# Performance work log

Measured on AMD Instinct MI355X. Metric: run time of the kernel, lower is better.

Reference implementation:

```python
import jax, jax.numpy as jnp
import numpy as np
from math import sqrt

RATIOS = [0.5, 1.0, 2.0]
SCALES = [128.0, 256.0, 512.0]
STRIDE = 16
NA = 9  # len(RATIOS) * len(SCALES)


def _anchor_template():
    # matches RPNHead.__init__: center at stride/2, w = s/sqrt(r), h = s*sqrt(r)
    t = np.zeros((NA, 4), np.float32)
    for ri, r in enumerate(RATIOS):
        for si, s in enumerate(SCALES):
            i = ri * len(RATIOS) + si
            sr = sqrt(r)
            t[i] = [STRIDE / 2.0, STRIDE / 2.0, s / sr, s * sr]
    return jnp.asarray(t)


def _conv(x, w, b, pad):
    y = jax.lax.conv_general_dilated(
        x, w, window_strides=(1, 1), padding=[(pad, pad), (pad, pad)],
        dimension_numbers=('NCHW', 'OIHW', 'NCHW'))
    return y + b[None, :, None, None]


def setup_inputs() -> dict:
    key = jax.random.key(0)
    ks = jax.random.split(key, 5)
    B, C, H, W = 8, 512, 64, 64
    return {
        'feature_maps': jax.random.normal(ks[0], (B, C, H, W), jnp.float32),
        'img_size': jnp.ones((B, 2), jnp.int32) * 1024,  # (width, height) per image
        'conv_w': jax.random.normal(ks[1], (512, 512, 3, 3), jnp.float32) * 0.01,
        'conv_b': jnp.zeros((512,), jnp.float32),
        'cls_w': jax.random.normal(ks[2], (2 * NA, 512, 1, 1), jnp.float32) * 0.01,
        'cls_b': jnp.zeros((2 * NA,), jnp.float32),
        'reg_w': jax.random.normal(ks[3], (4 * NA, 512, 1, 1), jnp.float32) * 0.01,
        'reg_b': jnp.zeros((4 * NA,), jnp.float32),
    }


def reference(feature_maps, img_size, conv_w, conv_b, cls_w, cls_b, reg_w, reg_b):
    f = jax.nn.relu(_conv(feature_maps, conv_w, conv_b, 1))  # [B,512,H,W]
    B, _, H, W = f.shape
    # heads, NCHW -> NHWC, split anchor dim
    cls = _conv(f, cls_w, cls_b, 0).transpose(0, 2, 3, 1).reshape(B, H, W, NA, 2)
    reg = _conv(f, reg_w, reg_b, 0).transpose(0, 2, 3, 1).reshape(B, H, W, NA, 4)

    # generate_anchors (eval mode: anchors_ignore stays zero)
    tmpl = _anchor_template()  # [NA,4] xywh
    gy, gx = jnp.meshgrid(jnp.arange(H), jnp.arange(W), indexing='ij')
    center = jnp.stack([gx, gy], axis=-1).astype(jnp.float32) * STRIDE  # [H,W,2] (x,y)
    axy = tmpl[None, None, :, :2] + center[:, :, None, :]               # [H,W,NA,2]
    awh = jnp.broadcast_to(tmpl[None, None, :, 2:], (H, W, NA, 2))
    anchors = jnp.concatenate([axy, awh], axis=-1).reshape(-1, 4)       # [A,4]

    A = anchors.shape[0]
    reg = reg.reshape(B, A, 4)
    cls_scores = cls.reshape(B, A, 2)

    # anchor2bbox: inverse of the delta encoding in loss()
    ax, ay, aw, ah = anchors[:, 0], anchors[:, 1], anchors[:, 2], anchors[:, 3]
    px = ax[None, :] + reg[..., 0] * aw[None, :]
    py = ay[None, :] + reg[..., 1] * ah[None, :]
    pw = aw[None, :] * jnp.exp(reg[..., 2])
    ph = ah[None, :] * jnp.exp(reg[..., 3])
    imw = img_size[:, 0:1].astype(jnp.float32)
    imh = img_size[:, 1:2].astype(jnp.float32)
    x1 = jnp.clip(px - pw / 2, 0.0, imw)
    y1 = jnp.clip(py - ph / 2, 0.0, imh)
    x2 = jnp.clip(px + pw / 2, 0.0, imw)
    y2 = jnp.clip(py + ph / 2, 0.0, imh)
    proposals = jnp.stack([x1, y1, x2, y2], axis=-1)  # [B,A,4]

    anchors_ignore = jnp.zeros((B, A), jnp.int32)
    return (proposals, cls_scores, anchors_ignore)
```

## Files before the change

kernel.cpp:

```cpp
#include <hip/hip_runtime.h>
#include <hip/hip_bf16.h>
#include <stdint.h>

typedef __attribute__((ext_vector_type(4))) float f32x4;
typedef __attribute__((ext_vector_type(8))) short short8;

#define NB 8
#define NC 512
#define HP 66
#define WP 66
#define NPOS 32768
#define KTOT 4608
#define NKT 72

#define XP_ELEMS (NB*HP*WP*NC)
#define WR_ELEMS (NC*KTOT)
#define WC2_ELEMS (64*NC)
#define PROP_OFF 0
#define CLS_OFF  1179648
#define ANCH_OFF 1769472
#define A_PER_B  36864

__device__ __forceinline__ short bf16bits(float v) {
    __hip_bfloat16 b = __float2bfloat16(v);
    return *reinterpret_cast<short*>(&b);
}
__device__ __forceinline__ void gload16(const short* g, short* l) {
    __builtin_amdgcn_global_load_lds(
        (const __attribute__((address_space(1))) unsigned int*)g,
        (__attribute__((address_space(3))) unsigned int*)l, 16, 0, 0);
}
#define BARRIER() asm volatile("s_barrier" ::: "memory")
#define VMCNT4()  asm volatile("s_waitcnt vmcnt(4)" ::: "memory")
#define VMCNT0()  asm volatile("s_waitcnt vmcnt(0)" ::: "memory")

__global__ void prep_all(const float* __restrict__ x, const float* __restrict__ conv_w,
                         const float* __restrict__ cls_w, const float* __restrict__ reg_w,
                         short* __restrict__ Wr, short* __restrict__ Wc2,
                         short* __restrict__ Xp) {
    __shared__ float smem[4608];
    const int bid = blockIdx.x, tid = threadIdx.x;
    if (bid < 4096) {
        float (*t)[65] = (float(*)[65])smem;
        const int pb = bid & 63, cb = (bid >> 6) & 7, b = bid >> 9;
        const int tx = tid & 63, ty = tid >> 6;
        const float* src = x + ((size_t)(b*NC + cb*64))*4096 + pb*64;
#pragma unroll
        for (int r = 0; r < 16; ++r) {
            int ch = ty + r*4;
            t[ch][tx] = src[(size_t)ch*4096 + tx];
        }
        __syncthreads();
#pragma unroll
        for (int rr = 0; rr < 2; ++rr) {
            int item = tid + rr*256;
            int pl = item >> 3, ck = item & 7;
            short8 v;
#pragma unroll
            for (int e = 0; e < 8; ++e) v[e] = bf16bits(t[ck*8+e][pl]);
            *(short8*)&Xp[((size_t)((b*HP + pb + 1)*WP) + (pl + 1))*NC + cb*64 + ck*8] = v;
        }
    } else if (bid < 4608) {
        const int o = bid - 4096;
        const float* src = conv_w + (size_t)o*4608;
        for (int i = tid; i < 4608; i += 256) smem[i] = src[i];
        __syncthreads();
#pragma unroll
        for (int k = 0; k < 9; ++k)
#pragma unroll
            for (int c = 0; c < 2; ++c) {
                int ci = tid + c*256;
                Wr[(size_t)o*4608 + k*512 + ci] = bf16bits(smem[ci*9 + k]);
            }
    } else {
        const int m = bid - 4608;
        if (m < 128) {
            int t = m*256 + tid;
            int row = t >> 9, ci = t & 511;
            float v = 0.f;
            if (row < 18)      v = cls_w[row*NC + ci];
            else if (row < 54) v = reg_w[(row-18)*NC + ci];
            Wc2[t] = bf16bits(v);
        } else {
            int idx = (m-128)*256 + tid;
            int b = idx / 16640;
            int rem = idx - b*16640;
            int r = rem >> 6, g = rem & 63;
            int h, w;
            if      (r < 66)  { h = 0;       w = r; }
            else if (r < 132) { h = 65;      w = r - 66; }
            else if (r < 196) { h = r - 131; w = 0; }
            else              { h = r - 195; w = 65; }
            short8 z = (short8){0,0,0,0,0,0,0,0};
            *(short8*)&Xp[((size_t)((b*HP + h)*WP) + w)*NC + g*8] = z;
        }
    }
}

__launch_bounds__(512, 2)
__global__ void conv_fused(const short* __restrict__ Xp, const short* __restrict__ Wr,
                           const float* __restrict__ bias, const short* __restrict__ Wc2,
                           float* __restrict__ partial) {
    extern __shared__ short lds[];
    const int tid = threadIdx.x;
    const int lane = tid & 63, wv = tid >> 6;
    const int bid = blockIdx.x;
    const int wg = (bid & 7) * 32 + (bid >> 3);
    const int pbase  = (wg >> 1) * 256;
    const int cobase = (wg & 1) * 256;
    const int wm = wv >> 2, wn = wv & 3;

    const int g_data = (tid & 7) ^ ((tid >> 3) & 7);
    int abase[4], bbase[4];
#pragma unroll
    for (int q = 0; q < 4; ++q) {
        int p = pbase + q*64 + (tid >> 3);
        int b = p >> 12, h = (p >> 6) & 63, w = p & 63;
        abase[q] = ((b*HP + h)*WP + w)*NC + g_data*8;
        bbase[q] = (cobase + q*64 + (tid >> 3))*KTOT + g_data*8;
    }
    const int stoff = tid*8;

    const int l15 = lane & 15, l4 = lane >> 4, l7 = lane & 7;
    const int kidx0 = (l4 ^ l7) * 8;
    const int kidx1 = ((4 + l4) ^ l7) * 8;
    const int Aroff = wm*8192 + l15*64;
    const int Broff = 16384 + (wn>>1)*8192 + (wn&1)*4096 + l15*64;

    auto stageA = [&](int t, int hh) {
        int seg = t >> 3;
        int dh = seg / 3, dw = seg - dh*3;
        int off = (dh*WP + dw)*NC + (t & 7)*64;
        short* dst = lds + (t & 1)*32768 + hh*8192 + stoff;
        gload16(Xp + abase[hh*2+0] + off, dst);
        gload16(Xp + abase[hh*2+1] + off, dst + 4096);
    };
    auto stageB = [&](int t, int hh) {
        int off = t * 64;
        short* dst = lds + (t & 1)*32768 + 16384 + hh*8192 + stoff;
        gload16(Wr + bbase[hh*2+0] + off, dst);
        gload16(Wr + bbase[hh*2+1] + off, dst + 4096);
    };

    f32x4 acc[8][4];
#pragma unroll
    for (int i = 0; i < 8; ++i)
#pragma unroll
        for (int j = 0; j < 4; ++j) acc[i][j] = (f32x4){0.f,0.f,0.f,0.f};

    short8 af[2][2], bfr[4][2];
    auto readA = [&](int bufb, int i2) {
        const short* Ab = lds + bufb*32768 + Aroff;
#pragma unroll
        for (int ii = 0; ii < 2; ++ii) {
            af[ii][0] = *(const short8*)(Ab + (i2+ii)*1024 + kidx0);
            af[ii][1] = *(const short8*)(Ab + (i2+ii)*1024 + kidx1);
        }
    };
    auto readB = [&](int bufb) {
        const short* Bb = lds + bufb*32768 + Broff;
#pragma unroll
        for (int j = 0; j < 4; ++j) {
            bfr[j][0] = *(const short8*)(Bb + j*1024 + kidx0);
            bfr[j][1] = *(const short8*)(Bb + j*1024 + kidx1);
        }
    };
    auto mfmaQ = [&](int i2) {
        __builtin_amdgcn_s_setprio(1);
#pragma unroll
        for (int kk = 0; kk < 2; ++kk)
#pragma unroll
            for (int ii = 0; ii < 2; ++ii)
#pragma unroll
                for (int j = 0; j < 4; ++j)
                    acc[i2+ii][j] = __builtin_amdgcn_mfma_f32_16x16x32_bf16(
                        af[ii][kk], bfr[j][kk], acc[i2+ii][j], 0, 0, 0);
        __builtin_amdgcn_s_setprio(0);
    };

    stageB(0,0); stageB(0,1); stageA(0,0); stageA(0,1); stageB(1,0); stageB(1,1);
    VMCNT4(); BARRIER();

    for (int it = 0; it < 36; ++it) {
        const int t1 = 2*it+1, t2 = 2*it+2, t3 = 2*it+3;
        const bool s2 = (t2 < NKT), s3 = (t3 < NKT);
        readB(0); readA(0, 0);
        stageA(t1, 0);
        BARRIER(); mfmaQ(0); BARRIER();
        readA(0, 2);
        stageA(t1, 1);
        BARRIER(); mfmaQ(2); BARRIER();
        readA(0, 4);
        if (s2) stageB(t2, 0);
        BARRIER(); mfmaQ(4); BARRIER();
        readA(0, 6);
        if (s2) stageB(t2, 1);
        BARRIER(); mfmaQ(6);
        if (s2) { VMCNT4(); } else { VMCNT0(); }
        BARRIER();
        readB(1); readA(1, 0);
        if (s2) stageA(t2, 0);
        BARRIER(); mfmaQ(0); BARRIER();
        readA(1, 2);
        if (s2) stageA(t2, 1);
        BARRIER(); mfmaQ(2); BARRIER();
        readA(1, 4);
        if (s3) stageB(t3, 0);
        BARRIER(); mfmaQ(4); BARRIER();
        readA(1, 6);
        if (s3) stageB(t3, 1);
        BARRIER(); mfmaQ(6);
        if (s3) { VMCNT4(); } else { VMCNT0(); }
        BARRIER();
    }
    __syncthreads();

#pragma unroll
    for (int j = 0; j < 4; ++j) {
        const int ch = wn*64 + j*16 + l15;
        const float bb = bias[cobase + ch];
        const int g = ch >> 3, e = ch & 7;
#pragma unroll
        for (int i = 0; i < 8; ++i) {
#pragma unroll
            for (int r = 0; r < 4; ++r) {
                const int pos = wm*128 + i*16 + l4*4 + r;
                float v = acc[i][j][r] + bb;
                v = v > 0.f ? v : 0.f;
                const int slot = (g & 24) | ((g ^ pos) & 7);
                lds[pos*256 + slot*8 + e] = bf16bits(v);
            }
        }
    }
    __syncthreads();

    f32x4 acc2[2][4];
#pragma unroll
    for (int i2 = 0; i2 < 2; ++i2)
#pragma unroll
        for (int j2 = 0; j2 < 4; ++j2) acc2[i2][j2] = (f32x4){0.f,0.f,0.f,0.f};
    const int hbase = wv*32;
#pragma unroll
    for (int kk = 0; kk < 8; ++kk) {
        short8 b2[4];
#pragma unroll
        for (int j2 = 0; j2 < 4; ++j2)
            b2[j2] = *(const short8*)&Wc2[(size_t)(j2*16 + l15)*NC + cobase + kk*32 + l4*8];
#pragma unroll
        for (int i2 = 0; i2 < 2; ++i2) {
            const int pos = hbase + i2*16 + l15;
            const int g = kk*4 + l4;
            const int slot = (g & 24) | ((g ^ pos) & 7);
            short8 a2 = *(const short8*)&lds[pos*256 + slot*8];
#pragma unroll
            for (int j2 = 0; j2 < 4; ++j2)
                acc2[i2][j2] = __builtin_amdgcn_mfma_f32_16x16x32_bf16(
                    a2, b2[j2], acc2[i2][j2], 0, 0, 0);
        }
    }

    const int half = wg & 1;
    float* pdst = partial + ((size_t)half*NPOS + pbase + hbase)*64;
#pragma unroll
    for (int i2 = 0; i2 < 2; ++i2)
#pragma unroll
        for (int j2 = 0; j2 < 4; ++j2)
#pragma unroll
            for (int r = 0; r < 4; ++r)
                pdst[(i2*16 + l4*4 + r)*64 + j2*16 + l15] = acc2[i2][j2][r];
}

__device__ const float AW_T[9] = {
    181.01933598375618f, 362.03867196751236f, 724.0773439350247f,
    128.f, 256.f, 512.f,
    90.50966799187809f, 181.01933598375618f, 362.03867196751236f };
__device__ const float AH_T[9] = {
    90.50966799187809f, 181.01933598375618f, 362.03867196751236f,
    128.f, 256.f, 512.f,
    181.01933598375618f, 362.03867196751236f, 724.0773439350247f };

__launch_bounds__(256)
__global__ void combine_decode(const float* __restrict__ partial,
                               const float* __restrict__ cls_b, const float* __restrict__ reg_b,
                               const int* __restrict__ img, float* __restrict__ out) {
    __shared__ float sm[64*65];
    const int tid = threadIdx.x;
    const int p0 = blockIdx.x * 64;
    const float4* pa = (const float4*)partial;
#pragma unroll
    for (int q = 0; q < 4; ++q) {
        int idx = tid + q*256;
        int pl = idx >> 4, n4 = idx & 15;
        float4 a = pa[(size_t)(p0 + pl)*16 + n4];
        float4 b = pa[(size_t)(NPOS + p0 + pl)*16 + n4];
        sm[pl*65 + n4*4 + 0] = a.x + b.x;
        sm[pl*65 + n4*4 + 1] = a.y + b.y;
        sm[pl*65 + n4*4 + 2] = a.z + b.z;
        sm[pl*65 + n4*4 + 3] = a.w + b.w;
    }
    __syncthreads();

    for (int item = tid; item < 576; item += 256) {
        int pl = item / 9, a = item - pl*9;
        int p = p0 + pl;
        int b = p >> 12, h = (p >> 6) & 63, w = p & 63;
        float c0 = sm[pl*65 + a*2 + 0] + cls_b[a*2 + 0];
        float c1 = sm[pl*65 + a*2 + 1] + cls_b[a*2 + 1];
        float r0 = sm[pl*65 + 18 + a*4 + 0] + reg_b[a*4 + 0];
        float r1 = sm[pl*65 + 18 + a*4 + 1] + reg_b[a*4 + 1];
        float r2 = sm[pl*65 + 18 + a*4 + 2] + reg_b[a*4 + 2];
        float r3 = sm[pl*65 + 18 + a*4 + 3] + reg_b[a*4 + 3];
        float aw = AW_T[a], ah = AH_T[a];
        float ax = 8.f + 16.f*w, ay = 8.f + 16.f*h;
        float px = ax + r0*aw,  py = ay + r1*ah;
        float pw = aw*__expf(r2), ph = ah*__expf(r3);
        float imw = (float)img[b*2 + 0], imh = (float)img[b*2 + 1];
        float x1 = fminf(fmaxf(px - 0.5f*pw, 0.f), imw);
        float y1 = fminf(fmaxf(py - 0.5f*ph, 0.f), imh);
        float x2 = fminf(fmaxf(px + 0.5f*pw, 0.f), imw);
        float y2 = fminf(fmaxf(py + 0.5f*ph, 0.f), imh);
        int ag = (h*64 + w)*9 + a;
        float4* prop = (float4*)(out + PROP_OFF + ((size_t)b*A_PER_B + ag)*4);
        *prop = make_float4(x1, y1, x2, y2);
        float2* cs = (float2*)(out + CLS_OFF + ((size_t)b*A_PER_B + ag)*2);
        *cs = make_float2(c0, c1);
        out[ANCH_OFF + (size_t)b*A_PER_B + ag] = 0.0f;
    }
}

extern "C" void kernel_launch(void* const* d_in, const int* in_sizes, int n_in,
                              void* d_out, int out_size, void* d_ws, size_t ws_size,
                              hipStream_t stream) {
    const float* x      = (const float*)d_in[0];
    const int*   img    = (const int*)  d_in[1];
    const float* conv_w = (const float*)d_in[2];
    const float* conv_b = (const float*)d_in[3];
    const float* cls_w  = (const float*)d_in[4];
    const float* cls_b  = (const float*)d_in[5];
    const float* reg_w  = (const float*)d_in[6];
    const float* reg_b  = (const float*)d_in[7];
    float* out = (float*)d_out;

    short* Xp      = (short*)d_ws;
    short* Wr      = Xp  + XP_ELEMS;
    short* Wc2     = Wr  + WR_ELEMS;
    float* partial = (float*)(Wc2 + WC2_ELEMS);

    prep_all<<<5256, 256, 0, stream>>>(x, conv_w, cls_w, reg_w, Wr, Wc2, Xp);

    hipFuncSetAttribute((const void*)conv_fused,
                        hipFuncAttributeMaxDynamicSharedMemorySize, 131072);
    conv_fused<<<256, 512, 131072, stream>>>(Xp, Wr, conv_b, Wc2, partial);
    combine_decode<<<NPOS/64, 256, 0, stream>>>(partial, cls_b, reg_b, img, out);
}
```

Baseline: 248.1 us.

## Merge prep, conv and decode into one cooperative persistent kernel with grid syncs

Replaces the three separate launches (prep, fused conv, combine/decode) with a single cooperative kernel of 256 workgroups that runs the three phases back to back, separated by grid-wide syncs. The prep phase is reworked so each 512-thread block runs two 256-thread teams over the transpose and weight-reorder jobs, and the input reads become float4 loads. The aim is to remove launch overhead and the gaps between kernels. In exchange, prep and decode now run on only 256 large workgroups at low occupancy, and the kernel pays for two grid barriers.

```diff
diff --git a/kernel.cpp b/kernel.cpp
--- a/kernel.cpp
+++ b/kernel.cpp
@@ -1,6 +1,9 @@
 #include <hip/hip_runtime.h>
 #include <hip/hip_bf16.h>
+#include <hip/hip_cooperative_groups.h>
 #include <stdint.h>
+
+namespace cg = cooperative_groups;
 
 typedef __attribute__((ext_vector_type(4))) float f32x4;
 typedef __attribute__((ext_vector_type(8))) short short8;
@@ -20,6 +23,7 @@
 #define CLS_OFF  1179648
 #define ANCH_OFF 1769472
 #define A_PER_B  36864
+#define TSTRIDE  4672
 
 __device__ __forceinline__ short bf16bits(float v) {
     __hip_bfloat16 b = __float2bfloat16(v);
@@ -34,55 +38,86 @@
 #define VMCNT4()  asm volatile("s_waitcnt vmcnt(4)" ::: "memory")
 #define VMCNT0()  asm volatile("s_waitcnt vmcnt(0)" ::: "memory")
 
-__global__ void prep_all(const float* __restrict__ x, const float* __restrict__ conv_w,
-                         const float* __restrict__ cls_w, const float* __restrict__ reg_w,
-                         short* __restrict__ Wr, short* __restrict__ Wc2,
-                         short* __restrict__ Xp) {
-    __shared__ float smem[4608];
-    const int bid = blockIdx.x, tid = threadIdx.x;
-    if (bid < 4096) {
-        float (*t)[65] = (float(*)[65])smem;
-        const int pb = bid & 63, cb = (bid >> 6) & 7, b = bid >> 9;
-        const int tx = tid & 63, ty = tid >> 6;
-        const float* src = x + ((size_t)(b*NC + cb*64))*4096 + pb*64;
-#pragma unroll
-        for (int r = 0; r < 16; ++r) {
-            int ch = ty + r*4;
-            t[ch][tx] = src[(size_t)ch*4096 + tx];
-        }
-        __syncthreads();
-#pragma unroll
-        for (int rr = 0; rr < 2; ++rr) {
-            int item = tid + rr*256;
-            int pl = item >> 3, ck = item & 7;
-            short8 v;
-#pragma unroll
-            for (int e = 0; e < 8; ++e) v[e] = bf16bits(t[ck*8+e][pl]);
-            *(short8*)&Xp[((size_t)((b*HP + pb + 1)*WP) + (pl + 1))*NC + cb*64 + ck*8] = v;
-        }
-    } else if (bid < 4608) {
-        const int o = bid - 4096;
-        const float* src = conv_w + (size_t)o*4608;
-        for (int i = tid; i < 4608; i += 256) smem[i] = src[i];
-        __syncthreads();
-#pragma unroll
-        for (int k = 0; k < 9; ++k)
-#pragma unroll
-            for (int c = 0; c < 2; ++c) {
-                int ci = tid + c*256;
-                Wr[(size_t)o*4608 + k*512 + ci] = bf16bits(smem[ci*9 + k]);
+__device__ const float AW_T[9] = {
+    181.01933598375618f, 362.03867196751236f, 724.0773439350247f,
+    128.f, 256.f, 512.f,
+    90.50966799187809f, 181.01933598375618f, 362.03867196751236f };
+__device__ const float AH_T[9] = {
+    90.50966799187809f, 181.01933598375618f, 362.03867196751236f,
+    128.f, 256.f, 512.f,
+    181.01933598375618f, 362.03867196751236f, 724.0773439350247f };
+
+__launch_bounds__(512, 2)
+__global__ void mega(const float* __restrict__ x, const int* __restrict__ img,
+                     const float* __restrict__ conv_w, const float* __restrict__ bias,
+                     const float* __restrict__ cls_w, const float* __restrict__ cls_b,
+                     const float* __restrict__ reg_w, const float* __restrict__ reg_b,
+                     float* __restrict__ out, short* __restrict__ Xp,
+                     short* __restrict__ Wr, short* __restrict__ Wc2,
+                     float* __restrict__ partial) {
+    extern __shared__ short lds[];
+    cg::grid_group gg = cg::this_grid();
+    const int tid = threadIdx.x;
+    const int bid = blockIdx.x;
+
+    {
+        const int team = tid >> 8, ttid = tid & 255;
+        float* tsm = (float*)lds + team*TSTRIDE;
+        float (*t65)[65] = (float(*)[65])tsm;
+
+#pragma unroll 1
+        for (int r = 0; r < 8; ++r) {
+            const int job = bid*16 + r*2 + team;
+            const int pb = job & 63, cb = (job >> 6) & 7, b = job >> 9;
+            const float* src = x + ((size_t)(b*NC + cb*64))*4096 + pb*64;
+            const int w4 = ttid & 15, chb = ttid >> 4;
+#pragma unroll
+            for (int r2 = 0; r2 < 4; ++r2) {
+                int ch = r2*16 + chb;
+                float4 v = *(const float4*)(src + (size_t)ch*4096 + w4*4);
+                t65[ch][w4*4 + 0] = v.x;
+                t65[ch][w4*4 + 1] = v.y;
+                t65[ch][w4*4 + 2] = v.z;
+                t65[ch][w4*4 + 3] = v.w;
             }
-    } else {
-        const int m = bid - 4608;
-        if (m < 128) {
-            int t = m*256 + tid;
+            __syncthreads();
+#pragma unroll
+            for (int rr = 0; rr < 2; ++rr) {
+                int item = ttid + rr*256;
+                int pl = item >> 3, ck = item & 7;
+                short8 v;
+#pragma unroll
+                for (int e = 0; e < 8; ++e) v[e] = bf16bits(t65[ck*8+e][pl]);
+                *(short8*)&Xp[((size_t)((b*HP + pb + 1)*WP) + (pl + 1))*NC + cb*64 + ck*8] = v;
+            }
+            __syncthreads();
+        }
+
+        {
+            const int o = bid*2 + team;
+            const float4* src4 = (const float4*)(conv_w + (size_t)o*4608);
+            float4* tsm4 = (float4*)tsm;
+            for (int i = ttid; i < 1152; i += 256) tsm4[i] = src4[i];
+            __syncthreads();
+#pragma unroll
+            for (int k = 0; k < 9; ++k)
+#pragma unroll
+                for (int c = 0; c < 2; ++c) {
+                    int ci = ttid + c*256;
+                    Wr[(size_t)o*4608 + k*512 + ci] = bf16bits(tsm[ci*9 + k]);
+                }
+            __syncthreads();
+        }
+
+        if (bid < 64) {
+            int t = bid*512 + tid;
             int row = t >> 9, ci = t & 511;
             float v = 0.f;
             if (row < 18)      v = cls_w[row*NC + ci];
             else if (row < 54) v = reg_w[(row-18)*NC + ci];
             Wc2[t] = bf16bits(v);
-        } else {
-            int idx = (m-128)*256 + tid;
+        }
+        for (int idx = bid*512 + tid; idx < 133120; idx += 131072) {
             int b = idx / 16640;
             int rem = idx - b*16640;
             int r = rem >> 6, g = rem & 63;
@@ -95,16 +130,10 @@
             *(short8*)&Xp[((size_t)((b*HP + h)*WP) + w)*NC + g*8] = z;
         }
     }
-}
-
-__launch_bounds__(512, 2)
-__global__ void conv_fused(const short* __restrict__ Xp, const short* __restrict__ Wr,
-                           const float* __restrict__ bias, const short* __restrict__ Wc2,
-                           float* __restrict__ partial) {
-    extern __shared__ short lds[];
-    const int tid = threadIdx.x;
+    __threadfence();
+    gg.sync();
+
     const int lane = tid & 63, wv = tid >> 6;
-    const int bid = blockIdx.x;
     const int wg = (bid & 7) * 32 + (bid >> 3);
     const int pbase  = (wg >> 1) * 256;
     const int cobase = (wg & 1) * 256;
@@ -268,63 +297,53 @@
 #pragma unroll
             for (int r = 0; r < 4; ++r)
                 pdst[(i2*16 + l4*4 + r)*64 + j2*16 + l15] = acc2[i2][j2][r];
-}
-
-__device__ const float AW_T[9] = {
-    181.01933598375618f, 362.03867196751236f, 724.0773439350247f,
-    128.f, 256.f, 512.f,
-    90.50966799187809f, 181.01933598375618f, 362.03867196751236f };
-__device__ const float AH_T[9] = {
-    90.50966799187809f, 181.01933598375618f, 362.03867196751236f,
-    128.f, 256.f, 512.f,
-    181.01933598375618f, 362.03867196751236f, 724.0773439350247f };
-
-__launch_bounds__(256)
-__global__ void combine_decode(const float* __restrict__ partial,
-                               const float* __restrict__ cls_b, const float* __restrict__ reg_b,
-                               const int* __restrict__ img, float* __restrict__ out) {
-    __shared__ float sm[64*65];
-    const int tid = threadIdx.x;
-    const int p0 = blockIdx.x * 64;
-    const float4* pa = (const float4*)partial;
-#pragma unroll
-    for (int q = 0; q < 4; ++q) {
-        int idx = tid + q*256;
-        int pl = idx >> 4, n4 = idx & 15;
-        float4 a = pa[(size_t)(p0 + pl)*16 + n4];
-        float4 b = pa[(size_t)(NPOS + p0 + pl)*16 + n4];
-        sm[pl*65 + n4*4 + 0] = a.x + b.x;
-        sm[pl*65 + n4*4 + 1] = a.y + b.y;
-        sm[pl*65 + n4*4 + 2] = a.z + b.z;
-        sm[pl*65 + n4*4 + 3] = a.w + b.w;
-    }
-    __syncthreads();
-
-    for (int item = tid; item < 576; item += 256) {
-        int pl = item / 9, a = item - pl*9;
-        int p = p0 + pl;
-        int b = p >> 12, h = (p >> 6) & 63, w = p & 63;
-        float c0 = sm[pl*65 + a*2 + 0] + cls_b[a*2 + 0];
-        float c1 = sm[pl*65 + a*2 + 1] + cls_b[a*2 + 1];
-        float r0 = sm[pl*65 + 18 + a*4 + 0] + reg_b[a*4 + 0];
-        float r1 = sm[pl*65 + 18 + a*4 + 1] + reg_b[a*4 + 1];
-        float r2 = sm[pl*65 + 18 + a*4 + 2] + reg_b[a*4 + 2];
-        float r3 = sm[pl*65 + 18 + a*4 + 3] + reg_b[a*4 + 3];
-        float aw = AW_T[a], ah = AH_T[a];
-        float ax = 8.f + 16.f*w, ay = 8.f + 16.f*h;
-        float px = ax + r0*aw,  py = ay + r1*ah;
-        float pw = aw*__expf(r2), ph = ah*__expf(r3);
-        float imw = (float)img[b*2 + 0], imh = (float)img[b*2 + 1];
-        float x1 = fminf(fmaxf(px - 0.5f*pw, 0.f), imw);
-        float y1 = fminf(fmaxf(py - 0.5f*ph, 0.f), imh);
-        float x2 = fminf(fmaxf(px + 0.5f*pw, 0.f), imw);
-        float y2 = fminf(fmaxf(py + 0.5f*ph, 0.f), imh);
-        int ag = (h*64 + w)*9 + a;
-        float4* prop = (float4*)(out + PROP_OFF + ((size_t)b*A_PER_B + ag)*4);
-        *prop = make_float4(x1, y1, x2, y2);
-        float2* cs = (float2*)(out + CLS_OFF + ((size_t)b*A_PER_B + ag)*2);
-        *cs = make_float2(c0, c1);
-        out[ANCH_OFF + (size_t)b*A_PER_B + ag] = 0.0f;
+
+    __threadfence();
+    gg.sync();
+
+    {
+        float* sm = (float*)lds;
+        const int dp0 = bid * 128;
+        const float4* pa = (const float4*)partial;
+#pragma unroll
+        for (int q = 0; q < 4; ++q) {
+            int idx = tid + q*512;
+            int pl = idx >> 4, n4 = idx & 15;
+            float4 a = pa[(size_t)(dp0 + pl)*16 + n4];
+            float4 b = pa[(size_t)(NPOS + dp0 + pl)*16 + n4];
+            sm[pl*65 + n4*4 + 0] = a.x + b.x;
+            sm[pl*65 + n4*4 + 1] = a.y + b.y;
+            sm[pl*65 + n4*4 + 2] = a.z + b.z;
+            sm[pl*65 + n4*4 + 3] = a.w + b.w;
+        }
+        __syncthreads();
+
+        for (int item = tid; item < 1152; item += 512) {
+            int pl = item / 9, a = item - pl*9;
+            int p = dp0 + pl;
+            int b = p >> 12, h = (p >> 6) & 63, w = p & 63;
+            float c0 = sm[pl*65 + a*2 + 0] + cls_b[a*2 + 0];
+            float c1 = sm[pl*65 + a*2 + 1] + cls_b[a*2 + 1];
+            float r0 = sm[pl*65 + 18 + a*4 + 0] + reg_b[a*4 + 0];
+            float r1 = sm[pl*65 + 18 + a*4 + 1] + reg_b[a*4 + 1];
+            float r2 = sm[pl*65 + 18 + a*4 + 2] + reg_b[a*4 + 2];
+            float r3 = sm[pl*65 + 18 + a*4 + 3] + reg_b[a*4 + 3];
+            float aw = AW_T[a], ah = AH_T[a];
+            float ax = 8.f + 16.f*w, ay = 8.f + 16.f*h;
+            float px = ax + r0*aw,  py = ay + r1*ah;
+            float pw = aw*__expf(r2), ph = ah*__expf(r3);
+            float imw = (float)img[b*2 + 0], imh = (float)img[b*2 + 1];
+            float x1 = fminf(fmaxf(px - 0.5f*pw, 0.f), imw);
+            float y1 = fminf(fmaxf(py - 0.5f*ph, 0.f), imh);
+            float x2 = fminf(fmaxf(px + 0.5f*pw, 0.f), imw);
+            float y2 = fminf(fmaxf(py + 0.5f*ph, 0.f), imh);
+            int ag = (h*64 + w)*9 + a;
+            float4* prop = (float4*)(out + PROP_OFF + ((size_t)b*A_PER_B + ag)*4);
+            *prop = make_float4(x1, y1, x2, y2);
+            float2* cs = (float2*)(out + CLS_OFF + ((size_t)b*A_PER_B + ag)*2);
+            *cs = make_float2(c0, c1);
+            out[ANCH_OFF + (size_t)b*A_PER_B + ag] = 0.0f;
+        }
     }
 }
 
@@ -346,10 +365,12 @@
     short* Wc2     = Wr  + WR_ELEMS;
     float* partial = (float*)(Wc2 + WC2_ELEMS);
 
-    prep_all<<<5256, 256, 0, stream>>>(x, conv_w, cls_w, reg_w, Wr, Wc2, Xp);
-
-    hipFuncSetAttribute((const void*)conv_fused,
+    hipFuncSetAttribute((const void*)mega,
                         hipFuncAttributeMaxDynamicSharedMemorySize, 131072);
-    conv_fused<<<256, 512, 131072, stream>>>(Xp, Wr, conv_b, Wc2, partial);
-    combine_decode<<<NPOS/64, 256, 0, stream>>>(partial, cls_b, reg_b, img, out);
+    void* args[] = {(void*)&x, (void*)&img, (void*)&conv_w, (void*)&conv_b,
+                    (void*)&cls_w, (void*)&cls_b, (void*)&reg_w, (void*)&reg_b,
+                    (void*)&out, (void*)&Xp, (void*)&Wr, (void*)&Wc2,
+                    (void*)&partial};
+    hipLaunchCooperativeKernel((const void*)mega, dim3(256), dim3(512),
+                               args, 131072, stream);
 }
```

Measured after the change: 455.0 us. +83.4%, slower.
